# Kernel tuning notes

Measured on AMD Instinct MI355X. Metric: run time of the kernel, lower is better.

## Reference

```python
import jax, jax.numpy as jnp
import numpy as np

B = 65536   # batch (number of parallel envs)
HID = 64    # GRU hidden / FC width
ACT = 3     # action count


def setup_inputs() -> dict:
    key = jax.random.key(0)
    ks = iter(jax.random.split(key, 64))

    def rn(shape, s=0.1):
        return jax.random.normal(next(ks), shape, dtype=jnp.float32) * s

    inp = {
        "obs": jax.random.uniform(next(ks), (B, 7, 7, 3), dtype=jnp.float32, maxval=10.0),
        "memory": rn((B, 4 * HID), 1.0),
        "conv_w1": rn((16, 3, 2, 2)), "conv_b1": rn((16,)),
        "conv_w2": rn((32, 16, 2, 2)), "conv_b2": rn((32,)),
        "conv_w3": rn((64, 32, 2, 2)), "conv_b3": rn((64,)),
    }
    for g in ("g1", "g2"):
        for l in (0, 1):
            inp[f"{g}_wih{l}"] = rn((3 * HID, HID))
            inp[f"{g}_whh{l}"] = rn((3 * HID, HID))
            inp[f"{g}_bih{l}"] = rn((3 * HID,))
            inp[f"{g}_bhh{l}"] = rn((3 * HID,))
    inp.update({
        "actor_w1": rn((HID, HID)), "actor_b1": rn((HID,)),
        "actor_w2": rn((ACT, HID)), "actor_b2": rn((ACT,)),
        "critic_w1": rn((HID, HID)), "critic_b1": rn((HID,)),
        "critic_w2": rn((1, HID)), "critic_b2": rn((1,)),
    })
    return inp


def _conv(x, w, b):
    # NCHW, OIHW, VALID, stride 1 (matches nn.Conv2d defaults)
    y = jax.lax.conv_general_dilated(x, w, (1, 1), 'VALID',
                                     dimension_numbers=('NCHW', 'OIHW', 'NCHW'))
    return y + b[None, :, None, None]


def _maxpool2(x):
    return jax.lax.reduce_window(x, -jnp.inf, jax.lax.max,
                                 (1, 1, 2, 2), (1, 1, 2, 2), 'VALID')


def _gru_cell(x, h, wih, whh, bih, bhh):
    # PyTorch GRU cell math (gate order: r, z, n)
    gi = x @ wih.T + bih
    gh = h @ whh.T + bhh
    i_r, i_z, i_n = jnp.split(gi, 3, axis=-1)
    h_r, h_z, h_n = jnp.split(gh, 3, axis=-1)
    r = jax.nn.sigmoid(i_r + h_r)
    z = jax.nn.sigmoid(i_z + h_z)
    n = jnp.tanh(i_n + r * h_n)
    return (1.0 - z) * n + z * h


def reference(obs, memory, conv_w1, conv_b1, conv_w2, conv_b2, conv_w3, conv_b3,
              g1_wih0, g1_whh0, g1_bih0, g1_bhh0, g1_wih1, g1_whh1, g1_bih1, g1_bhh1,
              g2_wih0, g2_whh0, g2_bih0, g2_bhh0, g2_wih1, g2_whh1, g2_bih1, g2_bhh1,
              actor_w1, actor_b1, actor_w2, actor_b2,
              critic_w1, critic_b1, critic_w2, critic_b2):
    bsz = memory.shape[0]
    # obs.transpose(1,3).transpose(2,3): NHWC -> NCHW
    x = jnp.transpose(obs, (0, 3, 1, 2))
    x = jax.nn.relu(_conv(x, conv_w1, conv_b1))   # [B,16,6,6]
    x = _maxpool2(x)                              # [B,16,3,3]
    x = jax.nn.relu(_conv(x, conv_w2, conv_b2))   # [B,32,2,2]
    x = jax.nn.relu(_conv(x, conv_w3, conv_b3))   # [B,64,1,1]
    x = x.reshape(bsz, -1)                        # [B,64]

    h1 = memory[:, :2 * HID].reshape(bsz, 2, HID)
    h2 = memory[:, 2 * HID:].reshape(bsz, 2, HID)

    # single-timestep 2-layer GRU #1
    inp = x
    h1_new = []
    for l, (wih, whh, bih, bhh) in enumerate([(g1_wih0, g1_whh0, g1_bih0, g1_bhh0),
                                              (g1_wih1, g1_whh1, g1_bih1, g1_bhh1)]):
        inp = _gru_cell(inp, h1[:, l], wih, whh, bih, bhh)
        h1_new.append(inp)
    mem1 = jnp.stack(h1_new, axis=1).reshape(bsz, 2 * HID)

    # single-timestep 2-layer GRU #2 (input = GRU1 top-layer output)
    h2_new = []
    for l, (wih, whh, bih, bhh) in enumerate([(g2_wih0, g2_whh0, g2_bih0, g2_bhh0),
                                              (g2_wih1, g2_whh1, g2_bih1, g2_bhh1)]):
        inp = _gru_cell(inp, h2[:, l], wih, whh, bih, bhh)
        h2_new.append(inp)
    mem2 = jnp.stack(h2_new, axis=1).reshape(bsz, 2 * HID)

    embedding = inp  # GRU2 top-layer output, [B,64]

    logits = jax.nn.relu(embedding @ actor_w1.T + actor_b1) @ actor_w2.T + actor_b2
    log_probs = jax.nn.log_softmax(logits, axis=1)          # Categorical(logits=log_softmax)
    value = (jax.nn.relu(embedding @ critic_w1.T + critic_b1) @ critic_w2.T + critic_b2)[:, 0]
    memory_out = jnp.concatenate([mem1, mem2], axis=1)      # [B,256]
    return (log_probs, value, memory_out)
```

## Files before the change

kernel.cpp:

```cpp
#include <hip/hip_runtime.h>

#define BATCH 65536
#define NT 256
#define NTG 512
#define MFMA __builtin_amdgcn_mfma_f32_16x16x32_bf16

typedef short bf16x8 __attribute__((ext_vector_type(8)));
typedef float f32x4 __attribute__((ext_vector_type(4)));
typedef unsigned short u16x8 __attribute__((ext_vector_type(8)));
typedef unsigned short u16x4 __attribute__((ext_vector_type(4)));

__device__ __forceinline__ float sigmoidf_(float x) { return 1.0f / (1.0f + __expf(-x)); }
__device__ __forceinline__ float tanhf_(float x) { return 2.0f / (1.0f + __expf(-2.0f * x)) - 1.0f; }
__device__ __forceinline__ unsigned short f2b(float f) {
  union { float f; unsigned int u; } v; v.f = f;
  unsigned int r = (v.u + 0x7FFFu + ((v.u >> 16) & 1u)) >> 16;
  return (unsigned short)r;
}
__device__ __forceinline__ float b2f(unsigned short u) {
  return __uint_as_float(((unsigned int)u) << 16);
}
__device__ __forceinline__ bf16x8 cvt8(float4 a, float4 b) {
  union { unsigned short u[8]; bf16x8 v; } t;
  t.u[0] = f2b(a.x); t.u[1] = f2b(a.y); t.u[2] = f2b(a.z); t.u[3] = f2b(a.w);
  t.u[4] = f2b(b.x); t.u[5] = f2b(b.y); t.u[6] = f2b(b.z); t.u[7] = f2b(b.w);
  return t.v;
}

#define OSTR 149
#define PSTR 146
__global__ __launch_bounds__(NT) void k_front(
    const float* __restrict__ obs, const float* __restrict__ w1,
    const float* __restrict__ b1, const float* __restrict__ w2,
    const float* __restrict__ b2, unsigned short* __restrict__ c2b,
    const float* __restrict__ W0, const float* __restrict__ W1,
    const float* __restrict__ W2, const float* __restrict__ W3,
    const float* __restrict__ W4, const float* __restrict__ W5,
    const float* __restrict__ W6, const float* __restrict__ W7,
    const float* __restrict__ bi0, const float* __restrict__ bi1,
    const float* __restrict__ bi2, const float* __restrict__ bi3,
    const float* __restrict__ bh0, const float* __restrict__ bh1,
    const float* __restrict__ bh2, const float* __restrict__ bh3,
    const float* __restrict__ aw1, const float* __restrict__ cw1,
    const float* __restrict__ w3s,
    unsigned short* __restrict__ wsW, unsigned short* __restrict__ wsH,
    unsigned short* __restrict__ wsW3, float* __restrict__ wsB) {
  const int tid = threadIdx.x;
  const int b = blockIdx.x;

  if (b >= 1024) {
    const int pb = b - 1024;
    const int y = pb / 48;
    const int i = (pb % 48) * NT + tid;
    if (y < 8) {
      if (i >= 12288) return;
      const float* src = (y == 0) ? W0 : (y == 1) ? W1 : (y == 2) ? W2 : (y == 3) ? W3
                       : (y == 4) ? W4 : (y == 5) ? W5 : (y == 6) ? W6 : W7;
      const int c = y >> 1, p = y & 1;
      const int j = i >> 6, k = i & 63;
      const int g = j >> 6, jrow = j & 63;
      const int jt = jrow >> 4, r16i = jrow & 15;
      const int kseg = k >> 5, kgv = (k & 31) >> 3, e = k & 7;
      const int lane = kgv * 16 + r16i;
      const int q = g * 4 + p * 2 + kseg;
      wsW[c * 24576 + ((jt * 12 + q) * 64 + lane) * 8 + e] = f2b(src[i]);
    } else if (y == 8) {
      if (i < 4096) wsH[i] = f2b(aw1[i]);
    } else if (y == 9) {
      if (i < 4096) wsH[4096 + i] = f2b(cw1[i]);
    } else if (y == 10) {
      if (i < 8192) wsW3[i] = f2b(w3s[i]);
    } else {
      const int c = y - 11;
      if (i < 256) {
        const float* bi = (c == 0) ? bi0 : (c == 1) ? bi1 : (c == 2) ? bi2 : bi3;
        const float* bh = (c == 0) ? bh0 : (c == 1) ? bh1 : (c == 2) ? bh2 : bh3;
        const int j = i & 63, g = i >> 6;
        float v = (g == 0) ? bi[j] + bh[j]
                : (g == 1) ? bi[64 + j] + bh[64 + j]
                : (g == 2) ? bi[128 + j] : bh[128 + j];
        wsB[c * 256 + i] = v;
      }
    }
    return;
  }

  __shared__ unsigned short obs_b[64 * OSTR];
  __shared__ unsigned short pooled[64 * PSTR];
  const int lane = tid & 63;
  const int wave = tid >> 6;
  const int m_base = b * 64;

  {
    const float4* src = (const float4*)(obs + (size_t)m_base * 147);
#pragma unroll 1
    for (int i = tid; i < 2352; i += NT) {
      const float4 v = src[i];
      int idx = i * 4;
      int s = idx / 147;
      int c = idx - s * 147;
      obs_b[s * OSTR + c] = f2b(v.x);
      if (++c == 147) { c = 0; ++s; } obs_b[s * OSTR + c] = f2b(v.y);
      if (++c == 147) { c = 0; ++s; } obs_b[s * OSTR + c] = f2b(v.z);
      if (++c == 147) { c = 0; ++s; } obs_b[s * OSTR + c] = f2b(v.w);
    }
  }
  __syncthreads();

  if (wave < 3) {
    const int ph = wave, s = lane;
    float r[3][21];
#pragma unroll
    for (int rr = 0; rr < 3; ++rr)
#pragma unroll
      for (int i = 0; i < 21; ++i) r[rr][i] = b2f(obs_b[s * OSTR + (2 * ph + rr) * 21 + i]);
#pragma unroll 1
    for (int oc = 0; oc < 16; ++oc) {
      float wv[12];
#pragma unroll
      for (int i = 0; i < 12; ++i) wv[i] = w1[oc * 12 + i];
      const float bias = b1[oc];
#pragma unroll
      for (int pw = 0; pw < 3; ++pw) {
        float m = 0.0f;
#pragma unroll
        for (int dh = 0; dh < 2; ++dh)
#pragma unroll
          for (int dw = 0; dw < 2; ++dw) {
            float acc = bias;
#pragma unroll
            for (int kh = 0; kh < 2; ++kh)
#pragma unroll
              for (int kw = 0; kw < 2; ++kw)
#pragma unroll
                for (int c = 0; c < 3; ++c)
                  acc += r[dh + kh][(2 * pw + dw + kw) * 3 + c] * wv[c * 4 + kh * 2 + kw];
            m = fmaxf(m, fmaxf(acc, 0.0f));
          }
        pooled[s * PSTR + oc * 9 + ph * 3 + pw] = f2b(m);
      }
    }
  }
  __syncthreads();

  {
    const int g = wave, s = lane;
    const int ocb = g * 8;
    float acc[8][4];
#pragma unroll
    for (int u = 0; u < 8; ++u) {
      const float bb = b2[ocb + u];
      acc[u][0] = bb; acc[u][1] = bb; acc[u][2] = bb; acc[u][3] = bb;
    }
#pragma unroll 1
    for (int ic = 0; ic < 16; ++ic) {
      float p9[9];
#pragma unroll
      for (int p = 0; p < 9; ++p) p9[p] = b2f(pooled[s * PSTR + ic * 9 + p]);
#pragma unroll
      for (int u = 0; u < 8; ++u) {
        float w[4];
#pragma unroll
        for (int i = 0; i < 4; ++i) w[i] = w2[((ocb + u) * 16 + ic) * 4 + i];
#pragma unroll
        for (int oh = 0; oh < 2; ++oh)
#pragma unroll
          for (int ow = 0; ow < 2; ++ow)
            acc[u][oh * 2 + ow] += p9[(oh + 0) * 3 + (ow + 0)] * w[0] +
                                   p9[(oh + 0) * 3 + (ow + 1)] * w[1] +
                                   p9[(oh + 1) * 3 + (ow + 0)] * w[2] +
                                   p9[(oh + 1) * 3 + (ow + 1)] * w[3];
      }
    }
    unsigned short ob[32];
#pragma unroll
    for (int u = 0; u < 8; ++u)
#pragma unroll
      for (int p = 0; p < 4; ++p) ob[u * 4 + p] = f2b(fmaxf(acc[u][p], 0.0f));
#pragma unroll
    for (int i = 0; i < 4; ++i)
      *(u16x8*)(c2b + (size_t)(m_base + s) * 128 + g * 32 + 8 * i) = *(const u16x8*)(ob + 8 * i);
  }
}

#define XSTR 88
__global__ __launch_bounds__(NTG, 4) void k_gru(
    const unsigned short* __restrict__ c2b,
    const float* __restrict__ memF,
    const unsigned short* __restrict__ wsW,
    const unsigned short* __restrict__ wsW3,
    const float* __restrict__ wsB,
    const unsigned short* __restrict__ wsH,
    const float* __restrict__ b3,
    const float* __restrict__ ab1, const float* __restrict__ cb1,
    const float* __restrict__ aw2, const float* __restrict__ ab2,
    const float* __restrict__ cw2, const float* __restrict__ cb2,
    float* __restrict__ out) {
  __shared__ unsigned short wlds[24576];
  __shared__ unsigned short xls[128 * XSTR];
  const int tid = threadIdx.x;
  const int lane = tid & 63;
  const int wave = tid >> 6;
  const int r16 = lane & 15;
  const int kg = lane >> 4;
  const int wbase = wave * 16;
  const int m_base = blockIdx.x * 128 + wbase;
  float* outMem = out + (size_t)4 * BATCH;

  float4 wst[6];
  {
    const float4* wsrc = (const float4*)wsW;
#pragma unroll
    for (int r = 0; r < 6; ++r) wst[r] = wsrc[r * NTG + tid];
  }
  bf16x8 a0[4];
  {
    const unsigned short* ap = c2b + (size_t)(m_base + r16) * 128 + kg * 8;
#pragma unroll
    for (int f = 0; f < 4; ++f) a0[f] = *(const bf16x8*)(ap + f * 32);
  }
  float4 hraw[4];
  {
    const float* hp = memF + (size_t)(m_base + r16) * 256 + kg * 8;
    hraw[0] = *(const float4*)(hp);
    hraw[1] = *(const float4*)(hp + 4);
    hraw[2] = *(const float4*)(hp + 32);
    hraw[3] = *(const float4*)(hp + 36);
  }

#pragma unroll
  for (int n = 0; n < 4; ++n) {
    const unsigned short* bp = wsW3 + (size_t)(n * 16 + r16) * 128 + kg * 8;
    f32x4 q0 = (f32x4)(0.0f);
#pragma unroll
    for (int f = 0; f < 4; ++f) {
      bf16x8 bb = *(const bf16x8*)(bp + f * 32);
      q0 = MFMA(bb, a0[f], q0, 0, 0, 0);
    }
    const f32x4 b4 = *(const f32x4*)(b3 + n * 16 + kg * 4);
    u16x4 xo;
#pragma unroll
    for (int q = 0; q < 4; ++q) xo[q] = f2b(fmaxf(q0[q] + b4[q], 0.0f));
    *(u16x4*)(xls + (wbase + r16) * XSTR + n * 16 + kg * 4) = xo;
  }
  {
    float4* wd = (float4*)wlds;
#pragma unroll
    for (int r = 0; r < 6; ++r) wd[r * NTG + tid] = wst[r];
  }
  __syncthreads();

#pragma unroll 1
  for (int c = 0; c < 4; ++c) {
    const int co = c * 64;
    const float* bcp = wsB + c * 256;
    bf16x8 ax0, ax1, ah0, ah1;
    {
      const unsigned short* xp = xls + (wbase + r16) * XSTR + kg * 8;
      ax0 = *(const bf16x8*)(xp);
      ax1 = *(const bf16x8*)(xp + 32);
    }
    ah0 = cvt8(make_float4(hraw[0].x, hraw[0].y, hraw[0].z, hraw[0].w),
               make_float4(hraw[1].x, hraw[1].y, hraw[1].z, hraw[1].w));
    ah1 = cvt8(make_float4(hraw[2].x, hraw[2].y, hraw[2].z, hraw[2].w),
               make_float4(hraw[3].x, hraw[3].y, hraw[3].z, hraw[3].w));
    if (c < 3) {
      const float* hp = memF + (size_t)(m_base + r16) * 256 + (c + 1) * 64 + kg * 8;
      hraw[0] = *(const float4*)(hp);
      hraw[1] = *(const float4*)(hp + 4);
      hraw[2] = *(const float4*)(hp + 32);
      hraw[3] = *(const float4*)(hp + 36);
    }
    const unsigned short* wl = wlds + lane * 8;
#pragma unroll 1
    for (int jt = 0; jt < 4; ++jt) {
      const unsigned short* wjt = wl + jt * 6144;
      bf16x8 xr0 = *(const bf16x8*)(wjt);
      bf16x8 xr1 = *(const bf16x8*)(wjt + 512);
      bf16x8 hr0 = *(const bf16x8*)(wjt + 1024);
      bf16x8 hr1 = *(const bf16x8*)(wjt + 1536);
      bf16x8 xz0 = *(const bf16x8*)(wjt + 2048);
      bf16x8 xz1 = *(const bf16x8*)(wjt + 2560);
      bf16x8 hz0 = *(const bf16x8*)(wjt + 3072);
      bf16x8 hz1 = *(const bf16x8*)(wjt + 3584);
      bf16x8 xn0 = *(const bf16x8*)(wjt + 4096);
      bf16x8 xn1 = *(const bf16x8*)(wjt + 4608);
      bf16x8 hn0 = *(const bf16x8*)(wjt + 5120);
      bf16x8 hn1 = *(const bf16x8*)(wjt + 5632);
      f32x4 sr = (f32x4)(0.0f), sz = (f32x4)(0.0f), sn = (f32x4)(0.0f), tn = (f32x4)(0.0f);
      sr = MFMA(xr0, ax0, sr, 0, 0, 0);
      sr = MFMA(xr1, ax1, sr, 0, 0, 0);
      sr = MFMA(hr0, ah0, sr, 0, 0, 0);
      sr = MFMA(hr1, ah1, sr, 0, 0, 0);
      sz = MFMA(xz0, ax0, sz, 0, 0, 0);
      sz = MFMA(xz1, ax1, sz, 0, 0, 0);
      sz = MFMA(hz0, ah0, sz, 0, 0, 0);
      sz = MFMA(hz1, ah1, sz, 0, 0, 0);
      sn = MFMA(xn0, ax0, sn, 0, 0, 0);
      sn = MFMA(xn1, ax1, sn, 0, 0, 0);
      tn = MFMA(hn0, ah0, tn, 0, 0, 0);
      tn = MFMA(hn1, ah1, tn, 0, 0, 0);
      const int jb = jt * 16 + kg * 4;
      const f32x4 ho4 = *(const f32x4*)(memF + (size_t)(m_base + r16) * 256 + co + jb);
      const f32x4 rb4 = *(const f32x4*)(bcp + jb);
      const f32x4 zb4 = *(const f32x4*)(bcp + 64 + jb);
      const f32x4 ib4 = *(const f32x4*)(bcp + 128 + jb);
      const f32x4 hb4 = *(const f32x4*)(bcp + 192 + jb);
      f32x4 nhv;
      u16x4 xo;
#pragma unroll
      for (int q = 0; q < 4; ++q) {
        const float rg = sigmoidf_(sr[q] + rb4[q]);
        const float zg = sigmoidf_(sz[q] + zb4[q]);
        const float ng = tanhf_((sn[q] + ib4[q]) + rg * (tn[q] + hb4[q]));
        const float nh = (1.0f - zg) * ng + zg * ho4[q];
        nhv[q] = nh;
        xo[q] = f2b(nh);
      }
      *(f32x4*)(outMem + (size_t)(m_base + r16) * 256 + co + jb) = nhv;
      *(u16x4*)(xls + (wbase + r16) * XSTR + jb) = xo;
    }
    if (c < 3) {
      __syncthreads();
      const float4* wsrc = (const float4*)(wsW + (size_t)(c + 1) * 24576);
      float4* wd = (float4*)wlds;
#pragma unroll
      for (int r = 0; r < 6; ++r) wd[r * NTG + tid] = wsrc[r * NTG + tid];
      __syncthreads();
    }
  }

  bf16x8 ex0, ex1;
  {
    const unsigned short* xp = xls + (wbase + r16) * XSTR + kg * 8;
    ex0 = *(const bf16x8*)(xp);
    ex1 = *(const bf16x8*)(xp + 32);
  }
  f32x4 ha[8];
#pragma unroll
  for (int n = 0; n < 8; ++n) ha[n] = (f32x4)(0.0f);
#pragma unroll
  for (int n = 0; n < 8; ++n) {
    const unsigned short* wp = wsH + (size_t)(n * 16 + r16) * 64 + kg * 8;
    bf16x8 b0 = *(const bf16x8*)(wp);
    bf16x8 b1 = *(const bf16x8*)(wp + 32);
    ha[n] = MFMA(b0, ex0, ha[n], 0, 0, 0);
    ha[n] = MFMA(b1, ex1, ha[n], 0, 0, 0);
  }
  float l0 = 0.0f, l1 = 0.0f, l2 = 0.0f, vv = 0.0f;
  const int jb0 = kg * 4;
#pragma unroll
  for (int t = 0; t < 4; ++t) {
    const f32x4 ba4 = *(const f32x4*)(ab1 + t * 16 + jb0);
    const f32x4 w0 = *(const f32x4*)(aw2 + t * 16 + jb0);
    const f32x4 w1v = *(const f32x4*)(aw2 + 64 + t * 16 + jb0);
    const f32x4 w2v = *(const f32x4*)(aw2 + 128 + t * 16 + jb0);
    const f32x4 bc4 = *(const f32x4*)(cb1 + t * 16 + jb0);
    const f32x4 wc4 = *(const f32x4*)(cw2 + t * 16 + jb0);
#pragma unroll
    for (int q = 0; q < 4; ++q) {
      const float av = fmaxf(ha[t][q] + ba4[q], 0.0f);
      const float cv = fmaxf(ha[t + 4][q] + bc4[q], 0.0f);
      l0 += av * w0[q]; l1 += av * w1v[q]; l2 += av * w2v[q];
      vv += cv * wc4[q];
    }
  }
  l0 += __shfl_xor(l0, 16); l0 += __shfl_xor(l0, 32);
  l1 += __shfl_xor(l1, 16); l1 += __shfl_xor(l1, 32);
  l2 += __shfl_xor(l2, 16); l2 += __shfl_xor(l2, 32);
  vv += __shfl_xor(vv, 16); vv += __shfl_xor(vv, 32);
  if (kg == 0) {
    const int sq = m_base + r16;
    const float g0 = l0 + ab2[0], g1 = l1 + ab2[1], g2 = l2 + ab2[2];
    const float mx = fmaxf(g0, fmaxf(g1, g2));
    const float lse = mx + __logf(__expf(g0 - mx) + __expf(g1 - mx) + __expf(g2 - mx));
    out[(size_t)sq * 3 + 0] = g0 - lse;
    out[(size_t)sq * 3 + 1] = g1 - lse;
    out[(size_t)sq * 3 + 2] = g2 - lse;
    out[(size_t)3 * BATCH + sq] = vv + cb2[0];
  }
}

extern "C" void kernel_launch(void* const* d_in, const int* in_sizes, int n_in,
                              void* d_out, int out_size, void* d_ws, size_t ws_size,
                              hipStream_t stream) {
  (void)in_sizes; (void)n_in; (void)out_size; (void)ws_size;
  const float* obs = (const float*)d_in[0];
  const float* mem = (const float*)d_in[1];
  const float* w1 = (const float*)d_in[2];
  const float* b1 = (const float*)d_in[3];
  const float* w2 = (const float*)d_in[4];
  const float* b2 = (const float*)d_in[5];
  const float* w3 = (const float*)d_in[6];
  const float* b3 = (const float*)d_in[7];
  const float* gw[16];
  for (int i = 0; i < 16; ++i) gw[i] = (const float*)d_in[8 + i];
  const float* aw1 = (const float*)d_in[24];
  const float* ab1 = (const float*)d_in[25];
  const float* aw2 = (const float*)d_in[26];
  const float* ab2 = (const float*)d_in[27];
  const float* cw1 = (const float*)d_in[28];
  const float* cb1 = (const float*)d_in[29];
  const float* cw2 = (const float*)d_in[30];
  const float* cb2 = (const float*)d_in[31];

  float* out = (float*)d_out;

  unsigned short* c2b = (unsigned short*)d_ws;
  unsigned short* wsW = c2b + (size_t)128 * BATCH;
  unsigned short* wsH = wsW + 98304;
  unsigned short* wsW3 = wsH + 8192;
  float* wsB = (float*)(wsW3 + 8192);

  hipLaunchKernelGGL(k_front, dim3(1024 + 720), dim3(NT), 0, stream,
                     obs, w1, b1, w2, b2, c2b,
                     gw[0], gw[1], gw[4], gw[5], gw[8], gw[9], gw[12], gw[13],
                     gw[2], gw[6], gw[10], gw[14],
                     gw[3], gw[7], gw[11], gw[15],
                     aw1, cw1, w3, wsW, wsH, wsW3, wsB);
  hipLaunchKernelGGL(k_gru, dim3(BATCH / 128), dim3(NTG), 0, stream,
                     c2b, mem, wsW, wsW3, wsB, wsH, b3,
                     ab1, cb1, aw2, ab2, cw2, cb2, out);
}
```

Before: 106.9 us.

## Fuse conv front-end into GRU kernel, keep conv2 output in LDS

Moves the conv1/pool/conv2 front-end from its own kernel into the GRU kernel, with 128 samples per block. The conv2 activations stay in shared memory instead of going through a global bf16 workspace. Weight preprocessing now runs as a small separate prep kernel. This removes the global write and read of the intermediate (16 MB round trip). In exchange the fused kernel uses more LDS and registers (~75 KB smem aliased), may lose occupancy, and the conv stage no longer overlaps with other work.

```diff
diff --git a/kernel.cpp b/kernel.cpp
--- a/kernel.cpp
+++ b/kernel.cpp
@@ -27,12 +27,7 @@
   return t.v;
 }
 
-#define OSTR 149
-#define PSTR 146
-__global__ __launch_bounds__(NT) void k_front(
-    const float* __restrict__ obs, const float* __restrict__ w1,
-    const float* __restrict__ b1, const float* __restrict__ w2,
-    const float* __restrict__ b2, unsigned short* __restrict__ c2b,
+__global__ __launch_bounds__(NT) void k_prep(
     const float* __restrict__ W0, const float* __restrict__ W1,
     const float* __restrict__ W2, const float* __restrict__ W3,
     const float* __restrict__ W4, const float* __restrict__ W5,
@@ -45,147 +40,48 @@
     const float* __restrict__ w3s,
     unsigned short* __restrict__ wsW, unsigned short* __restrict__ wsH,
     unsigned short* __restrict__ wsW3, float* __restrict__ wsB) {
-  const int tid = threadIdx.x;
-  const int b = blockIdx.x;
-
-  if (b >= 1024) {
-    const int pb = b - 1024;
-    const int y = pb / 48;
-    const int i = (pb % 48) * NT + tid;
-    if (y < 8) {
-      if (i >= 12288) return;
-      const float* src = (y == 0) ? W0 : (y == 1) ? W1 : (y == 2) ? W2 : (y == 3) ? W3
-                       : (y == 4) ? W4 : (y == 5) ? W5 : (y == 6) ? W6 : W7;
-      const int c = y >> 1, p = y & 1;
-      const int j = i >> 6, k = i & 63;
-      const int g = j >> 6, jrow = j & 63;
-      const int jt = jrow >> 4, r16i = jrow & 15;
-      const int kseg = k >> 5, kgv = (k & 31) >> 3, e = k & 7;
-      const int lane = kgv * 16 + r16i;
-      const int q = g * 4 + p * 2 + kseg;
-      wsW[c * 24576 + ((jt * 12 + q) * 64 + lane) * 8 + e] = f2b(src[i]);
-    } else if (y == 8) {
-      if (i < 4096) wsH[i] = f2b(aw1[i]);
-    } else if (y == 9) {
-      if (i < 4096) wsH[4096 + i] = f2b(cw1[i]);
-    } else if (y == 10) {
-      if (i < 8192) wsW3[i] = f2b(w3s[i]);
-    } else {
-      const int c = y - 11;
-      if (i < 256) {
-        const float* bi = (c == 0) ? bi0 : (c == 1) ? bi1 : (c == 2) ? bi2 : bi3;
-        const float* bh = (c == 0) ? bh0 : (c == 1) ? bh1 : (c == 2) ? bh2 : bh3;
-        const int j = i & 63, g = i >> 6;
-        float v = (g == 0) ? bi[j] + bh[j]
-                : (g == 1) ? bi[64 + j] + bh[64 + j]
-                : (g == 2) ? bi[128 + j] : bh[128 + j];
-        wsB[c * 256 + i] = v;
-      }
-    }
-    return;
-  }
-
-  __shared__ unsigned short obs_b[64 * OSTR];
-  __shared__ unsigned short pooled[64 * PSTR];
-  const int lane = tid & 63;
-  const int wave = tid >> 6;
-  const int m_base = b * 64;
-
-  {
-    const float4* src = (const float4*)(obs + (size_t)m_base * 147);
-#pragma unroll 1
-    for (int i = tid; i < 2352; i += NT) {
-      const float4 v = src[i];
-      int idx = i * 4;
-      int s = idx / 147;
-      int c = idx - s * 147;
-      obs_b[s * OSTR + c] = f2b(v.x);
-      if (++c == 147) { c = 0; ++s; } obs_b[s * OSTR + c] = f2b(v.y);
-      if (++c == 147) { c = 0; ++s; } obs_b[s * OSTR + c] = f2b(v.z);
-      if (++c == 147) { c = 0; ++s; } obs_b[s * OSTR + c] = f2b(v.w);
-    }
-  }
-  __syncthreads();
-
-  if (wave < 3) {
-    const int ph = wave, s = lane;
-    float r[3][21];
-#pragma unroll
-    for (int rr = 0; rr < 3; ++rr)
-#pragma unroll
-      for (int i = 0; i < 21; ++i) r[rr][i] = b2f(obs_b[s * OSTR + (2 * ph + rr) * 21 + i]);
-#pragma unroll 1
-    for (int oc = 0; oc < 16; ++oc) {
-      float wv[12];
-#pragma unroll
-      for (int i = 0; i < 12; ++i) wv[i] = w1[oc * 12 + i];
-      const float bias = b1[oc];
-#pragma unroll
-      for (int pw = 0; pw < 3; ++pw) {
-        float m = 0.0f;
-#pragma unroll
-        for (int dh = 0; dh < 2; ++dh)
-#pragma unroll
-          for (int dw = 0; dw < 2; ++dw) {
-            float acc = bias;
-#pragma unroll
-            for (int kh = 0; kh < 2; ++kh)
-#pragma unroll
-              for (int kw = 0; kw < 2; ++kw)
-#pragma unroll
-                for (int c = 0; c < 3; ++c)
-                  acc += r[dh + kh][(2 * pw + dw + kw) * 3 + c] * wv[c * 4 + kh * 2 + kw];
-            m = fmaxf(m, fmaxf(acc, 0.0f));
-          }
-        pooled[s * PSTR + oc * 9 + ph * 3 + pw] = f2b(m);
-      }
-    }
-  }
-  __syncthreads();
-
-  {
-    const int g = wave, s = lane;
-    const int ocb = g * 8;
-    float acc[8][4];
-#pragma unroll
-    for (int u = 0; u < 8; ++u) {
-      const float bb = b2[ocb + u];
-      acc[u][0] = bb; acc[u][1] = bb; acc[u][2] = bb; acc[u][3] = bb;
-    }
-#pragma unroll 1
-    for (int ic = 0; ic < 16; ++ic) {
-      float p9[9];
-#pragma unroll
-      for (int p = 0; p < 9; ++p) p9[p] = b2f(pooled[s * PSTR + ic * 9 + p]);
-#pragma unroll
-      for (int u = 0; u < 8; ++u) {
-        float w[4];
-#pragma unroll
-        for (int i = 0; i < 4; ++i) w[i] = w2[((ocb + u) * 16 + ic) * 4 + i];
-#pragma unroll
-        for (int oh = 0; oh < 2; ++oh)
-#pragma unroll
-          for (int ow = 0; ow < 2; ++ow)
-            acc[u][oh * 2 + ow] += p9[(oh + 0) * 3 + (ow + 0)] * w[0] +
-                                   p9[(oh + 0) * 3 + (ow + 1)] * w[1] +
-                                   p9[(oh + 1) * 3 + (ow + 0)] * w[2] +
-                                   p9[(oh + 1) * 3 + (ow + 1)] * w[3];
-      }
-    }
-    unsigned short ob[32];
-#pragma unroll
-    for (int u = 0; u < 8; ++u)
-#pragma unroll
-      for (int p = 0; p < 4; ++p) ob[u * 4 + p] = f2b(fmaxf(acc[u][p], 0.0f));
-#pragma unroll
-    for (int i = 0; i < 4; ++i)
-      *(u16x8*)(c2b + (size_t)(m_base + s) * 128 + g * 32 + 8 * i) = *(const u16x8*)(ob + 8 * i);
-  }
-}
-
+  const int y = blockIdx.y;
+  const int i = blockIdx.x * NT + threadIdx.x;
+  if (y < 8) {
+    if (i >= 12288) return;
+    const float* src = (y == 0) ? W0 : (y == 1) ? W1 : (y == 2) ? W2 : (y == 3) ? W3
+                     : (y == 4) ? W4 : (y == 5) ? W5 : (y == 6) ? W6 : W7;
+    const int c = y >> 1, p = y & 1;
+    const int j = i >> 6, k = i & 63;
+    const int g = j >> 6, jrow = j & 63;
+    const int jt = jrow >> 4, r16i = jrow & 15;
+    const int kseg = k >> 5, kgv = (k & 31) >> 3, e = k & 7;
+    const int lane = kgv * 16 + r16i;
+    const int q = g * 4 + p * 2 + kseg;
+    wsW[c * 24576 + ((jt * 12 + q) * 64 + lane) * 8 + e] = f2b(src[i]);
+  } else if (y == 8) {
+    if (i < 4096) wsH[i] = f2b(aw1[i]);
+  } else if (y == 9) {
+    if (i < 4096) wsH[4096 + i] = f2b(cw1[i]);
+  } else if (y == 10) {
+    if (i < 8192) wsW3[i] = f2b(w3s[i]);
+  } else {
+    const int c = y - 11;
+    if (i < 256) {
+      const float* bi = (c == 0) ? bi0 : (c == 1) ? bi1 : (c == 2) ? bi2 : bi3;
+      const float* bh = (c == 0) ? bh0 : (c == 1) ? bh1 : (c == 2) ? bh2 : bh3;
+      const int j = i & 63, g = i >> 6;
+      float v = (g == 0) ? bi[j] + bh[j]
+              : (g == 1) ? bi[64 + j] + bh[64 + j]
+              : (g == 2) ? bi[128 + j] : bh[128 + j];
+      wsB[c * 256 + i] = v;
+    }
+  }
+}
+
+#define OSTR 149
+#define PSTR 146
+#define CSTR 136
 #define XSTR 88
-__global__ __launch_bounds__(NTG, 4) void k_gru(
-    const unsigned short* __restrict__ c2b,
+__global__ __launch_bounds__(NTG, 4) void k_all(
+    const float* __restrict__ obs, const float* __restrict__ w1,
+    const float* __restrict__ b1, const float* __restrict__ w2,
+    const float* __restrict__ b2,
     const float* __restrict__ memF,
     const unsigned short* __restrict__ wsW,
     const unsigned short* __restrict__ wsW3,
@@ -196,28 +92,124 @@
     const float* __restrict__ aw2, const float* __restrict__ ab2,
     const float* __restrict__ cw2, const float* __restrict__ cb2,
     float* __restrict__ out) {
-  __shared__ unsigned short wlds[24576];
-  __shared__ unsigned short xls[128 * XSTR];
+  __shared__ __align__(16) unsigned short smem[37760];
+  unsigned short* obs_b = smem;
+  unsigned short* pooled = smem + 19072;
+  unsigned short* c2l = smem;
+  unsigned short* wlds = smem;
+  unsigned short* xls = smem + 24576;
   const int tid = threadIdx.x;
   const int lane = tid & 63;
   const int wave = tid >> 6;
   const int r16 = lane & 15;
   const int kg = lane >> 4;
   const int wbase = wave * 16;
-  const int m_base = blockIdx.x * 128 + wbase;
+  const int blk_base = blockIdx.x * 128;
+  const int m_base = blk_base + wbase;
   float* outMem = out + (size_t)4 * BATCH;
 
+  {
+    const float4* src = (const float4*)(obs + (size_t)blk_base * 147);
+#pragma unroll 1
+    for (int i = tid; i < 4704; i += NTG) {
+      const float4 v = src[i];
+      int idx = i * 4;
+      int s = idx / 147;
+      int c = idx - s * 147;
+      obs_b[s * OSTR + c] = f2b(v.x);
+      if (++c == 147) { c = 0; ++s; } obs_b[s * OSTR + c] = f2b(v.y);
+      if (++c == 147) { c = 0; ++s; } obs_b[s * OSTR + c] = f2b(v.z);
+      if (++c == 147) { c = 0; ++s; } obs_b[s * OSTR + c] = f2b(v.w);
+    }
+  }
+  __syncthreads();
+
+  {
+    const int s = tid & 127;
+    const int ph = tid >> 7;
+    if (ph < 3) {
+      float r[3][21];
+#pragma unroll
+      for (int rr = 0; rr < 3; ++rr)
+#pragma unroll
+        for (int i = 0; i < 21; ++i) r[rr][i] = b2f(obs_b[s * OSTR + (2 * ph + rr) * 21 + i]);
+#pragma unroll 1
+      for (int oc = 0; oc < 16; ++oc) {
+        float wv[12];
+#pragma unroll
+        for (int i = 0; i < 12; ++i) wv[i] = w1[oc * 12 + i];
+        const float bias = b1[oc];
+#pragma unroll
+        for (int pw = 0; pw < 3; ++pw) {
+          float m = 0.0f;
+#pragma unroll
+          for (int dh = 0; dh < 2; ++dh)
+#pragma unroll
+            for (int dw = 0; dw < 2; ++dw) {
+              float acc = bias;
+#pragma unroll
+              for (int kh = 0; kh < 2; ++kh)
+#pragma unroll
+                for (int kw = 0; kw < 2; ++kw)
+#pragma unroll
+                  for (int c = 0; c < 3; ++c)
+                    acc += r[dh + kh][(2 * pw + dw + kw) * 3 + c] * wv[c * 4 + kh * 2 + kw];
+              m = fmaxf(m, fmaxf(acc, 0.0f));
+            }
+          pooled[s * PSTR + oc * 9 + ph * 3 + pw] = f2b(m);
+        }
+      }
+    }
+  }
+  __syncthreads();
+
+  {
+    const int s = tid & 127;
+    const int g = tid >> 7;
+    const int ocb = g * 8;
+    float acc[8][4];
+#pragma unroll
+    for (int u = 0; u < 8; ++u) {
+      const float bb = b2[ocb + u];
+      acc[u][0] = bb; acc[u][1] = bb; acc[u][2] = bb; acc[u][3] = bb;
+    }
+#pragma unroll 1
+    for (int ic = 0; ic < 16; ++ic) {
+      float p9[9];
+#pragma unroll
+      for (int p = 0; p < 9; ++p) p9[p] = b2f(pooled[s * PSTR + ic * 9 + p]);
+#pragma unroll
+      for (int u = 0; u < 8; ++u) {
+        float w[4];
+#pragma unroll
+        for (int i = 0; i < 4; ++i) w[i] = w2[((ocb + u) * 16 + ic) * 4 + i];
+#pragma unroll
+        for (int oh = 0; oh < 2; ++oh)
+#pragma unroll
+          for (int ow = 0; ow < 2; ++ow)
+            acc[u][oh * 2 + ow] += p9[(oh + 0) * 3 + (ow + 0)] * w[0] +
+                                   p9[(oh + 0) * 3 + (ow + 1)] * w[1] +
+                                   p9[(oh + 1) * 3 + (ow + 0)] * w[2] +
+                                   p9[(oh + 1) * 3 + (ow + 1)] * w[3];
+      }
+    }
+    unsigned short ob[32];
+#pragma unroll
+    for (int u = 0; u < 8; ++u)
+#pragma unroll
+      for (int p = 0; p < 4; ++p) ob[u * 4 + p] = f2b(fmaxf(acc[u][p], 0.0f));
+    __syncthreads();
+#pragma unroll
+    for (int i = 0; i < 4; ++i)
+      *(u16x8*)(c2l + s * CSTR + g * 32 + 8 * i) = *(const u16x8*)(ob + 8 * i);
+  }
+  __syncthreads();
+
   float4 wst[6];
   {
     const float4* wsrc = (const float4*)wsW;
 #pragma unroll
     for (int r = 0; r < 6; ++r) wst[r] = wsrc[r * NTG + tid];
-  }
-  bf16x8 a0[4];
-  {
-    const unsigned short* ap = c2b + (size_t)(m_base + r16) * 128 + kg * 8;
-#pragma unroll
-    for (int f = 0; f < 4; ++f) a0[f] = *(const bf16x8*)(ap + f * 32);
   }
   float4 hraw[4];
   {
@@ -227,22 +219,28 @@
     hraw[2] = *(const float4*)(hp + 32);
     hraw[3] = *(const float4*)(hp + 36);
   }
-
-#pragma unroll
-  for (int n = 0; n < 4; ++n) {
-    const unsigned short* bp = wsW3 + (size_t)(n * 16 + r16) * 128 + kg * 8;
-    f32x4 q0 = (f32x4)(0.0f);
-#pragma unroll
-    for (int f = 0; f < 4; ++f) {
-      bf16x8 bb = *(const bf16x8*)(bp + f * 32);
-      q0 = MFMA(bb, a0[f], q0, 0, 0, 0);
-    }
-    const f32x4 b4 = *(const f32x4*)(b3 + n * 16 + kg * 4);
-    u16x4 xo;
-#pragma unroll
-    for (int q = 0; q < 4; ++q) xo[q] = f2b(fmaxf(q0[q] + b4[q], 0.0f));
-    *(u16x4*)(xls + (wbase + r16) * XSTR + n * 16 + kg * 4) = xo;
-  }
+  {
+    bf16x8 a0[4];
+    const unsigned short* ap = c2l + (wbase + r16) * CSTR + kg * 8;
+#pragma unroll
+    for (int f = 0; f < 4; ++f) a0[f] = *(const bf16x8*)(ap + f * 32);
+#pragma unroll
+    for (int n = 0; n < 4; ++n) {
+      const unsigned short* bp = wsW3 + (size_t)(n * 16 + r16) * 128 + kg * 8;
+      f32x4 q0 = (f32x4)(0.0f);
+#pragma unroll
+      for (int f = 0; f < 4; ++f) {
+        bf16x8 bb = *(const bf16x8*)(bp + f * 32);
+        q0 = MFMA(bb, a0[f], q0, 0, 0, 0);
+      }
+      const f32x4 b4 = *(const f32x4*)(b3 + n * 16 + kg * 4);
+      u16x4 xo;
+#pragma unroll
+      for (int q = 0; q < 4; ++q) xo[q] = f2b(fmaxf(q0[q] + b4[q], 0.0f));
+      *(u16x4*)(xls + (wbase + r16) * XSTR + n * 16 + kg * 4) = xo;
+    }
+  }
+  __syncthreads();
   {
     float4* wd = (float4*)wlds;
 #pragma unroll
@@ -406,19 +404,17 @@
 
   float* out = (float*)d_out;
 
-  unsigned short* c2b = (unsigned short*)d_ws;
-  unsigned short* wsW = c2b + (size_t)128 * BATCH;
+  unsigned short* wsW = (unsigned short*)d_ws;
   unsigned short* wsH = wsW + 98304;
   unsigned short* wsW3 = wsH + 8192;
   float* wsB = (float*)(wsW3 + 8192);
 
-  hipLaunchKernelGGL(k_front, dim3(1024 + 720), dim3(NT), 0, stream,
-                     obs, w1, b1, w2, b2, c2b,
+  hipLaunchKernelGGL(k_prep, dim3(48, 15), dim3(NT), 0, stream,
                      gw[0], gw[1], gw[4], gw[5], gw[8], gw[9], gw[12], gw[13],
                      gw[2], gw[6], gw[10], gw[14],
                      gw[3], gw[7], gw[11], gw[15],
                      aw1, cw1, w3, wsW, wsH, wsW3, wsB);
-  hipLaunchKernelGGL(k_gru, dim3(BATCH / 128), dim3(NTG), 0, stream,
-                     c2b, mem, wsW, wsW3, wsB, wsH, b3,
+  hipLaunchKernelGGL(k_all, dim3(BATCH / 128), dim3(NTG), 0, stream,
+                     obs, w1, b1, w2, b2, mem, wsW, wsW3, wsB, wsH, b3,
                      ab1, cb1, aw2, ab2, cw2, cb2, out);
 }
```

Result: slower. 116.3 us (+8.8%).

## Process two 16-row M tiles per wave in GRU kernel to reuse weight fragments

Applied to the files above, without the earlier changes.

Halves the GRU kernel's block from 512 to 256 threads while each wave now handles 32 batch rows (two 16-row MFMA tiles) instead of 16. Each LDS weight fragment load and each conv3 weight load is reused across both tiles, halving LDS weight traffic per row. The cost is higher register pressure (doubled accumulators and activations, launch bounds now 256 threads with 2 blocks per CU) and fewer waves available to hide latency.

```diff
diff --git a/kernel.cpp b/kernel.cpp
--- a/kernel.cpp
+++ b/kernel.cpp
@@ -2,7 +2,6 @@
 
 #define BATCH 65536
 #define NT 256
-#define NTG 512
 #define MFMA __builtin_amdgcn_mfma_f32_16x16x32_bf16
 
 typedef short bf16x8 __attribute__((ext_vector_type(8)));
@@ -184,7 +183,7 @@
 }
 
 #define XSTR 88
-__global__ __launch_bounds__(NTG, 4) void k_gru(
+__global__ __launch_bounds__(NT, 2) void k_gru(
     const unsigned short* __restrict__ c2b,
     const float* __restrict__ memF,
     const unsigned short* __restrict__ wsW,
@@ -203,50 +202,52 @@
   const int wave = tid >> 6;
   const int r16 = lane & 15;
   const int kg = lane >> 4;
-  const int wbase = wave * 16;
+  const int wbase = wave * 32;
   const int m_base = blockIdx.x * 128 + wbase;
   float* outMem = out + (size_t)4 * BATCH;
 
-  float4 wst[6];
+  float4 wst[12];
   {
     const float4* wsrc = (const float4*)wsW;
 #pragma unroll
-    for (int r = 0; r < 6; ++r) wst[r] = wsrc[r * NTG + tid];
-  }
-  bf16x8 a0[4];
-  {
-    const unsigned short* ap = c2b + (size_t)(m_base + r16) * 128 + kg * 8;
-#pragma unroll
-    for (int f = 0; f < 4; ++f) a0[f] = *(const bf16x8*)(ap + f * 32);
-  }
-  float4 hraw[4];
-  {
-    const float* hp = memF + (size_t)(m_base + r16) * 256 + kg * 8;
-    hraw[0] = *(const float4*)(hp);
-    hraw[1] = *(const float4*)(hp + 4);
-    hraw[2] = *(const float4*)(hp + 32);
-    hraw[3] = *(const float4*)(hp + 36);
+    for (int r = 0; r < 12; ++r) wst[r] = wsrc[r * NT + tid];
+  }
+  bf16x8 a0[2][4];
+  float4 hraw[2][4];
+#pragma unroll
+  for (int Mt = 0; Mt < 2; ++Mt) {
+    const unsigned short* ap = c2b + (size_t)(m_base + Mt * 16 + r16) * 128 + kg * 8;
+#pragma unroll
+    for (int f = 0; f < 4; ++f) a0[Mt][f] = *(const bf16x8*)(ap + f * 32);
+    const float* hp = memF + (size_t)(m_base + Mt * 16 + r16) * 256 + kg * 8;
+    hraw[Mt][0] = *(const float4*)(hp);
+    hraw[Mt][1] = *(const float4*)(hp + 4);
+    hraw[Mt][2] = *(const float4*)(hp + 32);
+    hraw[Mt][3] = *(const float4*)(hp + 36);
   }
 
 #pragma unroll
   for (int n = 0; n < 4; ++n) {
     const unsigned short* bp = wsW3 + (size_t)(n * 16 + r16) * 128 + kg * 8;
-    f32x4 q0 = (f32x4)(0.0f);
-#pragma unroll
-    for (int f = 0; f < 4; ++f) {
-      bf16x8 bb = *(const bf16x8*)(bp + f * 32);
-      q0 = MFMA(bb, a0[f], q0, 0, 0, 0);
-    }
+    bf16x8 wb[4];
+#pragma unroll
+    for (int f = 0; f < 4; ++f) wb[f] = *(const bf16x8*)(bp + f * 32);
     const f32x4 b4 = *(const f32x4*)(b3 + n * 16 + kg * 4);
-    u16x4 xo;
-#pragma unroll
-    for (int q = 0; q < 4; ++q) xo[q] = f2b(fmaxf(q0[q] + b4[q], 0.0f));
-    *(u16x4*)(xls + (wbase + r16) * XSTR + n * 16 + kg * 4) = xo;
+#pragma unroll
+    for (int Mt = 0; Mt < 2; ++Mt) {
+      f32x4 q0 = (f32x4)(0.0f);
+#pragma unroll
+      for (int f = 0; f < 4; ++f) q0 = MFMA(wb[f], a0[Mt][f], q0, 0, 0, 0);
+      u16x4 xo;
+#pragma unroll
+      for (int q = 0; q < 4; ++q) xo[q] = f2b(fmaxf(q0[q] + b4[q], 0.0f));
+      *(u16x4*)(xls + (wbase + Mt * 16 + r16) * XSTR + n * 16 + kg * 4) = xo;
+    }
   }
   {
     float4* wd = (float4*)wlds;
 #pragma unroll
-    for (int r = 0; r < 6; ++r) wd[r * NTG + tid] = wst[r];
+    for (int r = 0; r < 12; ++r) wd[r * NT + tid] = wst[r];
   }
   __syncthreads();
 
@@ -254,22 +255,26 @@
   for (int c = 0; c < 4; ++c) {
     const int co = c * 64;
     const float* bcp = wsB + c * 256;
-    bf16x8 ax0, ax1, ah0, ah1;
-    {
-      const unsigned short* xp = xls + (wbase + r16) * XSTR + kg * 8;
-      ax0 = *(const bf16x8*)(xp);
-      ax1 = *(const bf16x8*)(xp + 32);
-    }
-    ah0 = cvt8(make_float4(hraw[0].x, hraw[0].y, hraw[0].z, hraw[0].w),
-               make_float4(hraw[1].x, hraw[1].y, hraw[1].z, hraw[1].w));
-    ah1 = cvt8(make_float4(hraw[2].x, hraw[2].y, hraw[2].z, hraw[2].w),
-               make_float4(hraw[3].x, hraw[3].y, hraw[3].z, hraw[3].w));
+    bf16x8 ax[2][2], ah[2][2];
+#pragma unroll
+    for (int Mt = 0; Mt < 2; ++Mt) {
+      const unsigned short* xp = xls + (wbase + Mt * 16 + r16) * XSTR + kg * 8;
+      ax[Mt][0] = *(const bf16x8*)(xp);
+      ax[Mt][1] = *(const bf16x8*)(xp + 32);
+      ah[Mt][0] = cvt8(make_float4(hraw[Mt][0].x, hraw[Mt][0].y, hraw[Mt][0].z, hraw[Mt][0].w),
+                       make_float4(hraw[Mt][1].x, hraw[Mt][1].y, hraw[Mt][1].z, hraw[Mt][1].w));
+      ah[Mt][1] = cvt8(make_float4(hraw[Mt][2].x, hraw[Mt][2].y, hraw[Mt][2].z, hraw[Mt][2].w),
+                       make_float4(hraw[Mt][3].x, hraw[Mt][3].y, hraw[Mt][3].z, hraw[Mt][3].w));
+    }
     if (c < 3) {
-      const float* hp = memF + (size_t)(m_base + r16) * 256 + (c + 1) * 64 + kg * 8;
-      hraw[0] = *(const float4*)(hp);
-      hraw[1] = *(const float4*)(hp + 4);
-      hraw[2] = *(const float4*)(hp + 32);
-      hraw[3] = *(const float4*)(hp + 36);
+#pragma unroll
+      for (int Mt = 0; Mt < 2; ++Mt) {
+        const float* hp = memF + (size_t)(m_base + Mt * 16 + r16) * 256 + (c + 1) * 64 + kg * 8;
+        hraw[Mt][0] = *(const float4*)(hp);
+        hraw[Mt][1] = *(const float4*)(hp + 4);
+        hraw[Mt][2] = *(const float4*)(hp + 32);
+        hraw[Mt][3] = *(const float4*)(hp + 36);
+      }
     }
     const unsigned short* wl = wlds + lane * 8;
 #pragma unroll 1
@@ -287,68 +292,85 @@
       bf16x8 xn1 = *(const bf16x8*)(wjt + 4608);
       bf16x8 hn0 = *(const bf16x8*)(wjt + 5120);
       bf16x8 hn1 = *(const bf16x8*)(wjt + 5632);
-      f32x4 sr = (f32x4)(0.0f), sz = (f32x4)(0.0f), sn = (f32x4)(0.0f), tn = (f32x4)(0.0f);
-      sr = MFMA(xr0, ax0, sr, 0, 0, 0);
-      sr = MFMA(xr1, ax1, sr, 0, 0, 0);
-      sr = MFMA(hr0, ah0, sr, 0, 0, 0);
-      sr = MFMA(hr1, ah1, sr, 0, 0, 0);
-      sz = MFMA(xz0, ax0, sz, 0, 0, 0);
-      sz = MFMA(xz1, ax1, sz, 0, 0, 0);
-      sz = MFMA(hz0, ah0, sz, 0, 0, 0);
-      sz = MFMA(hz1, ah1, sz, 0, 0, 0);
-      sn = MFMA(xn0, ax0, sn, 0, 0, 0);
-      sn = MFMA(xn1, ax1, sn, 0, 0, 0);
-      tn = MFMA(hn0, ah0, tn, 0, 0, 0);
-      tn = MFMA(hn1, ah1, tn, 0, 0, 0);
+      f32x4 sr[2], sz[2], sn[2], tn[2];
+#pragma unroll
+      for (int Mt = 0; Mt < 2; ++Mt) {
+        sr[Mt] = (f32x4)(0.0f); sz[Mt] = (f32x4)(0.0f);
+        sn[Mt] = (f32x4)(0.0f); tn[Mt] = (f32x4)(0.0f);
+      }
+#pragma unroll
+      for (int Mt = 0; Mt < 2; ++Mt) {
+        sr[Mt] = MFMA(xr0, ax[Mt][0], sr[Mt], 0, 0, 0);
+        sr[Mt] = MFMA(xr1, ax[Mt][1], sr[Mt], 0, 0, 0);
+        sr[Mt] = MFMA(hr0, ah[Mt][0], sr[Mt], 0, 0, 0);
+        sr[Mt] = MFMA(hr1, ah[Mt][1], sr[Mt], 0, 0, 0);
+        sz[Mt] = MFMA(xz0, ax[Mt][0], sz[Mt], 0, 0, 0);
+        sz[Mt] = MFMA(xz1, ax[Mt][1], sz[Mt], 0, 0, 0);
+        sz[Mt] = MFMA(hz0, ah[Mt][0], sz[Mt], 0, 0, 0);
+        sz[Mt] = MFMA(hz1, ah[Mt][1], sz[Mt], 0, 0, 0);
+        sn[Mt] = MFMA(xn0, ax[Mt][0], sn[Mt], 0, 0, 0);
+        sn[Mt] = MFMA(xn1, ax[Mt][1], sn[Mt], 0, 0, 0);
+        tn[Mt] = MFMA(hn0, ah[Mt][0], tn[Mt], 0, 0, 0);
+        tn[Mt] = MFMA(hn1, ah[Mt][1], tn[Mt], 0, 0, 0);
+      }
       const int jb = jt * 16 + kg * 4;
-      const f32x4 ho4 = *(const f32x4*)(memF + (size_t)(m_base + r16) * 256 + co + jb);
       const f32x4 rb4 = *(const f32x4*)(bcp + jb);
       const f32x4 zb4 = *(const f32x4*)(bcp + 64 + jb);
       const f32x4 ib4 = *(const f32x4*)(bcp + 128 + jb);
       const f32x4 hb4 = *(const f32x4*)(bcp + 192 + jb);
-      f32x4 nhv;
-      u16x4 xo;
-#pragma unroll
-      for (int q = 0; q < 4; ++q) {
-        const float rg = sigmoidf_(sr[q] + rb4[q]);
-        const float zg = sigmoidf_(sz[q] + zb4[q]);
-        const float ng = tanhf_((sn[q] + ib4[q]) + rg * (tn[q] + hb4[q]));
-        const float nh = (1.0f - zg) * ng + zg * ho4[q];
-        nhv[q] = nh;
-        xo[q] = f2b(nh);
-      }
-      *(f32x4*)(outMem + (size_t)(m_base + r16) * 256 + co + jb) = nhv;
-      *(u16x4*)(xls + (wbase + r16) * XSTR + jb) = xo;
+#pragma unroll
+      for (int Mt = 0; Mt < 2; ++Mt) {
+        const f32x4 ho4 = *(const f32x4*)(memF + (size_t)(m_base + Mt * 16 + r16) * 256 + co + jb);
+        f32x4 nhv;
+        u16x4 xo;
+#pragma unroll
+        for (int q = 0; q < 4; ++q) {
+          const float rg = sigmoidf_(sr[Mt][q] + rb4[q]);
+          const float zg = sigmoidf_(sz[Mt][q] + zb4[q]);
+          const float ng = tanhf_((sn[Mt][q] + ib4[q]) + rg * (tn[Mt][q] + hb4[q]));
+          const float nh = (1.0f - zg) * ng + zg * ho4[q];
+          nhv[q] = nh;
+          xo[q] = f2b(nh);
+        }
+        *(f32x4*)(outMem + (size_t)(m_base + Mt * 16 + r16) * 256 + co + jb) = nhv;
+        *(u16x4*)(xls + (wbase + Mt * 16 + r16) * XSTR + jb) = xo;
+      }
     }
     if (c < 3) {
       __syncthreads();
       const float4* wsrc = (const float4*)(wsW + (size_t)(c + 1) * 24576);
       float4* wd = (float4*)wlds;
 #pragma unroll
-      for (int r = 0; r < 6; ++r) wd[r * NTG + tid] = wsrc[r * NTG + tid];
+      for (int r = 0; r < 12; ++r) wd[r * NT + tid] = wsrc[r * NT + tid];
       __syncthreads();
     }
   }
 
-  bf16x8 ex0, ex1;
-  {
-    const unsigned short* xp = xls + (wbase + r16) * XSTR + kg * 8;
-    ex0 = *(const bf16x8*)(xp);
-    ex1 = *(const bf16x8*)(xp + 32);
-  }
-  f32x4 ha[8];
-#pragma unroll
-  for (int n = 0; n < 8; ++n) ha[n] = (f32x4)(0.0f);
+  bf16x8 ex[2][2];
+#pragma unroll
+  for (int Mt = 0; Mt < 2; ++Mt) {
+    const unsigned short* xp = xls + (wbase + Mt * 16 + r16) * XSTR + kg * 8;
+    ex[Mt][0] = *(const bf16x8*)(xp);
+    ex[Mt][1] = *(const bf16x8*)(xp + 32);
+  }
+  f32x4 ha[2][8];
+#pragma unroll
+  for (int Mt = 0; Mt < 2; ++Mt)
+#pragma unroll
+    for (int n = 0; n < 8; ++n) ha[Mt][n] = (f32x4)(0.0f);
 #pragma unroll
   for (int n = 0; n < 8; ++n) {
     const unsigned short* wp = wsH + (size_t)(n * 16 + r16) * 64 + kg * 8;
     bf16x8 b0 = *(const bf16x8*)(wp);
     bf16x8 b1 = *(const bf16x8*)(wp + 32);
-    ha[n] = MFMA(b0, ex0, ha[n], 0, 0, 0);
-    ha[n] = MFMA(b1, ex1, ha[n], 0, 0, 0);
-  }
-  float l0 = 0.0f, l1 = 0.0f, l2 = 0.0f, vv = 0.0f;
+#pragma unroll
+    for (int Mt = 0; Mt < 2; ++Mt) {
+      ha[Mt][n] = MFMA(b0, ex[Mt][0], ha[Mt][n], 0, 0, 0);
+      ha[Mt][n] = MFMA(b1, ex[Mt][1], ha[Mt][n], 0, 0, 0);
+    }
+  }
   const int jb0 = kg * 4;
+  float l0[2] = {0.0f, 0.0f}, l1[2] = {0.0f, 0.0f}, l2[2] = {0.0f, 0.0f}, vv[2] = {0.0f, 0.0f};
 #pragma unroll
   for (int t = 0; t < 4; ++t) {
     const f32x4 ba4 = *(const f32x4*)(ab1 + t * 16 + jb0);
@@ -358,26 +380,31 @@
     const f32x4 bc4 = *(const f32x4*)(cb1 + t * 16 + jb0);
     const f32x4 wc4 = *(const f32x4*)(cw2 + t * 16 + jb0);
 #pragma unroll
-    for (int q = 0; q < 4; ++q) {
-      const float av = fmaxf(ha[t][q] + ba4[q], 0.0f);
-      const float cv = fmaxf(ha[t + 4][q] + bc4[q], 0.0f);
-      l0 += av * w0[q]; l1 += av * w1v[q]; l2 += av * w2v[q];
-      vv += cv * wc4[q];
-    }
-  }
-  l0 += __shfl_xor(l0, 16); l0 += __shfl_xor(l0, 32);
-  l1 += __shfl_xor(l1, 16); l1 += __shfl_xor(l1, 32);
-  l2 += __shfl_xor(l2, 16); l2 += __shfl_xor(l2, 32);
-  vv += __shfl_xor(vv, 16); vv += __shfl_xor(vv, 32);
-  if (kg == 0) {
-    const int sq = m_base + r16;
-    const float g0 = l0 + ab2[0], g1 = l1 + ab2[1], g2 = l2 + ab2[2];
-    const float mx = fmaxf(g0, fmaxf(g1, g2));
-    const float lse = mx + __logf(__expf(g0 - mx) + __expf(g1 - mx) + __expf(g2 - mx));
-    out[(size_t)sq * 3 + 0] = g0 - lse;
-    out[(size_t)sq * 3 + 1] = g1 - lse;
-    out[(size_t)sq * 3 + 2] = g2 - lse;
-    out[(size_t)3 * BATCH + sq] = vv + cb2[0];
+    for (int Mt = 0; Mt < 2; ++Mt)
+#pragma unroll
+      for (int q = 0; q < 4; ++q) {
+        const float av = fmaxf(ha[Mt][t][q] + ba4[q], 0.0f);
+        const float cv = fmaxf(ha[Mt][t + 4][q] + bc4[q], 0.0f);
+        l0[Mt] += av * w0[q]; l1[Mt] += av * w1v[q]; l2[Mt] += av * w2v[q];
+        vv[Mt] += cv * wc4[q];
+      }
+  }
+#pragma unroll
+  for (int Mt = 0; Mt < 2; ++Mt) {
+    l0[Mt] += __shfl_xor(l0[Mt], 16); l0[Mt] += __shfl_xor(l0[Mt], 32);
+    l1[Mt] += __shfl_xor(l1[Mt], 16); l1[Mt] += __shfl_xor(l1[Mt], 32);
+    l2[Mt] += __shfl_xor(l2[Mt], 16); l2[Mt] += __shfl_xor(l2[Mt], 32);
+    vv[Mt] += __shfl_xor(vv[Mt], 16); vv[Mt] += __shfl_xor(vv[Mt], 32);
+    if (kg == 0) {
+      const int sq = m_base + Mt * 16 + r16;
+      const float g0 = l0[Mt] + ab2[0], g1 = l1[Mt] + ab2[1], g2 = l2[Mt] + ab2[2];
+      const float mx = fmaxf(g0, fmaxf(g1, g2));
+      const float lse = mx + __logf(__expf(g0 - mx) + __expf(g1 - mx) + __expf(g2 - mx));
+      out[(size_t)sq * 3 + 0] = g0 - lse;
+      out[(size_t)sq * 3 + 1] = g1 - lse;
+      out[(size_t)sq * 3 + 2] = g2 - lse;
+      out[(size_t)3 * BATCH + sq] = vv[Mt] + cb2[0];
+    }
   }
 }
 
@@ -418,7 +445,7 @@
                      gw[2], gw[6], gw[10], gw[14],
                      gw[3], gw[7], gw[11], gw[15],
                      aw1, cw1, w3, wsW, wsH, wsW3, wsB);
-  hipLaunchKernelGGL(k_gru, dim3(BATCH / 128), dim3(NTG), 0, stream,
+  hipLaunchKernelGGL(k_gru, dim3(BATCH / 128), dim3(NT), 0, stream,
                      c2b, mem, wsW, wsW3, wsB, wsH, b3,
                      ab1, cb1, aw2, ab2, cw2, cb2, out);
 }
```

New measurement: 101.4 us (median of 2 runs). 1.05x faster.
